# Kernel optimization log

Measured on AMD Instinct MI355X. Metric: run time of the kernel, lower is better.

The kernel has to match this reference:

```python
import jax, jax.numpy as jnp
import numpy as np

N_HEADS = 4

def setup_inputs() -> dict:
    key = jax.random.key(0)
    ks = jax.random.split(key, 9)
    B, C, H, W = 4, 256, 64, 64
    nh, hs = N_HEADS, C // N_HEADS
    s = 0.02
    return {
        "x": jax.random.normal(ks[0], (B, C, H, W), jnp.float32),
        "wq": jax.random.normal(ks[1], (C, C), jnp.float32) * s,
        "bq": jax.random.normal(ks[2], (C,), jnp.float32) * s,
        "wk": jax.random.normal(ks[3], (C, C), jnp.float32) * s,
        "bk": jax.random.normal(ks[4], (C,), jnp.float32) * s,
        "wv": jax.random.normal(ks[5], (C, C), jnp.float32) * s,
        "bv": jax.random.normal(ks[6], (C,), jnp.float32) * s,
        "rel_h": jax.random.normal(ks[7], (1, nh, hs, 1, H), jnp.float32),
        "rel_w": jax.random.normal(ks[8], (1, nh, hs, W, 1), jnp.float32),
    }

def reference(x, wq, bq, wk, bk, wv, bv, rel_h, rel_w):
    B, C, H, W = x.shape
    nh = N_HEADS
    hs = C // nh
    S = H * W

    def proj(w, b):
        # 1x1 conv == per-pixel linear over channels -> [B, C, H, W]
        y = jnp.einsum('oc,bchw->bohw', w, x) + b[None, :, None, None]
        # faithful to torch .view: flatten [C,H,W] row-major into [S, nh, hs]
        y = y.reshape(B, S, nh, hs)
        return y.transpose(0, 2, 1, 3)  # [B, nh, S, hs]

    q = proj(wq, bq)
    k = proj(wk, bk)
    v = proj(wv, bv)

    # content scores (NOTE: no 1/sqrt(d) scaling in BoT override)
    attn_content = jnp.einsum('bnqd,bnkd->bnqk', q, k)  # [B, nh, S, S]
    # learned relative position term: broadcast-add then flatten (w,h) order
    pos = (rel_h + rel_w).reshape(1, nh, hs, S)  # [1, nh, hs, S]
    attn_position = jnp.einsum('bnqd,ands->bnqs', q, pos)  # [B, nh, S, S]

    probs = jax.nn.softmax(attn_content + attn_position, axis=-1)
    ctx = jnp.einsum('bnqk,bnkd->bnqd', probs, v)  # [B, nh, S, hs]
    # faithful to torch: transpose(1,2) then view(B, C, width, height)
    out = ctx.transpose(0, 2, 1, 3).reshape(B, C, W, H)
    return out
```

## Files before the change

### kernel.cpp

```cpp
#include <hip/hip_runtime.h>
#include <hip/hip_bf16.h>
#include <stdint.h>
#include <math.h>

typedef __bf16 bf16_t;
typedef __bf16 bf16x8 __attribute__((ext_vector_type(8)));
typedef float  f32x4  __attribute__((ext_vector_type(4)));
typedef float  f32x16 __attribute__((ext_vector_type(16)));
typedef unsigned int u32;

#define S_SZ 4096
#define HS   64
#define OUT_B_STRIDE (256 * 64 * 64)
#define LOG2E 1.4426950408889634f

#define GLOAD_LDS(gsrc, ldst)                                                              \
    __builtin_amdgcn_global_load_lds((__attribute__((address_space(1))) void*)(void*)(gsrc), \
                                     (__attribute__((address_space(3))) void*)(void*)(ldst),  \
                                     16, 0, 0)

static __device__ __forceinline__ u32 pack2(__bf16 a, __bf16 b) {
    return (u32)__builtin_bit_cast(uint16_t, a) | ((u32)__builtin_bit_cast(uint16_t, b) << 16);
}

__global__ __launch_bounds__(256)
void prep_kernel(const float* __restrict__ wq, const float* __restrict__ wk,
                 const float* __restrict__ wv, const float* __restrict__ rel_h,
                 const float* __restrict__ rel_w,
                 bf16_t* __restrict__ Wh, bf16_t* __restrict__ Wl,
                 bf16_t* __restrict__ Rt)
{
    const int blk = blockIdx.x;
    if (blk < 48) {
        const int base = blk * 4096;
        #pragma unroll
        for (int i = 0; i < 16; ++i) {
            const int e = base + i * 256 + threadIdx.x;
            const int o = e >> 8, c = e & 255;
            const float* src = o < 256 ? wq : (o < 512 ? wk : wv);
            float v = src[(size_t)(o & 255) * 256 + c];
            if (o < 256) v *= LOG2E;
            __bf16 h = (__bf16)v;
            Wh[e] = h;
            Wl[e] = (__bf16)(v - (float)h);
        }
    } else {
        const int rb = blk - 48;
        const int n = rb >> 4, h2 = rb & 15;
        __shared__ float rh[4096], rw[4096];
        for (int i = threadIdx.x; i < 4096; i += 256) {
            rh[i] = rel_h[n * 4096 + i];
            rw[i] = rel_w[n * 4096 + i];
        }
        __syncthreads();
        bf16_t* Rp = Rt + ((size_t)n * 4096 + h2 * 256) * 64;
        const int d0 = (threadIdx.x & 7) * 8;
        const int ob = threadIdx.x >> 3;
        #pragma unroll
        for (int i = 0; i < 8; ++i) {
            const int o  = i * 32 + ob;
            const int ih = (o & 3) * 16 + h2;
            const int iw = o >> 2;
            bf16x8 rv;
            #pragma unroll
            for (int dd = 0; dd < 8; ++dd)
                rv[dd] = (bf16_t)(rh[(d0 + dd) * 64 + ih] + rw[(d0 + dd) * 64 + iw]);
            *(bf16x8*)(Rp + (size_t)o * 64 + d0) = rv;
        }
    }
}

__global__ __launch_bounds__(512, 2)
void proj_kernel(const float* __restrict__ x,
                 const bf16_t* __restrict__ Wh, const bf16_t* __restrict__ Wl,
                 const float* __restrict__ bq, const float* __restrict__ bk,
                 const float* __restrict__ bv, const bf16_t* __restrict__ Rt,
                 bf16_t* __restrict__ q_ws, bf16_t* __restrict__ k2_ws,
                 bf16_t* __restrict__ vt2_ws)
{
    const int bx = blockIdx.x;
    const int b  = bx >> 6;
    const int h  = bx & 63;
    const int p0 = h * 64;
    const int n  = h & 3;
    const int h2 = h >> 2;
    const int bn = b * 4 + n;
    const int tid = threadIdx.x;

    __shared__ __align__(16) char SM[65536];

    {
        const int cpair = tid & 127, pg = tid >> 7;
        const int c0 = cpair * 2;
        const float* x0 = x + ((size_t)b * 256 + c0) * 4096 + p0 + pg * 16;
        const int sub = (c0 >> 6) * 128;
        const int u   = (c0 >> 3) & 7;
        const int e2  = (c0 & 7) * 2;
        #pragma unroll
        for (int i4 = 0; i4 < 4; ++i4) {
            f32x4 ra = *(const f32x4*)(x0 + i4 * 4);
            f32x4 rb = *(const f32x4*)(x0 + 4096 + i4 * 4);
            #pragma unroll
            for (int i = 0; i < 4; ++i) {
                const int p = pg * 16 + i4 * 4 + i;
                __bf16 ha = (__bf16)ra[i], hb = (__bf16)rb[i];
                float  la = ra[i] - (float)ha, lb = rb[i] - (float)hb;
                const int off = p * 512 + sub + ((u ^ (p & 7)) * 16) + e2;
                *(u32*)(SM + off)         = pack2(ha, hb);
                *(u32*)(SM + 32768 + off) = pack2((__bf16)la, (__bf16)lb);
            }
        }
    }
    __syncthreads();

    const int wid = tid >> 6, lane = tid & 63, l31 = lane & 31, hi = lane >> 5;

    int obs[3], pjs[3];
    const bf16_t* whp[3];
    const bf16_t* wlp[3];
    #pragma unroll
    for (int j = 0; j < 3; ++j) {
        const int of = (wid * 3 + j) * 32;
        pjs[j] = of >> 8;
        obs[j] = of & 255;
        whp[j] = Wh + (size_t)(of + l31) * 256 + hi * 8;
        wlp[j] = Wl + (size_t)(of + l31) * 256 + hi * 8;
    }

    const char* XHp = SM + l31 * 512;
    const char* XLp = SM + 32768 + l31 * 512;

    f32x16 acc[3][2] = {};

    bf16x8 whC[3], wlC[3], whN[3], wlN[3];
    #pragma unroll
    for (int j = 0; j < 3; ++j) {
        whC[j] = *(const bf16x8*)(whp[j]);
        wlC[j] = *(const bf16x8*)(wlp[j]);
    }

    #pragma unroll
    for (int ks = 0; ks < 16; ++ks) {
        if (ks < 15) {
            #pragma unroll
            for (int j = 0; j < 3; ++j) {
                whN[j] = *(const bf16x8*)(whp[j] + (ks + 1) * 16);
                wlN[j] = *(const bf16x8*)(wlp[j] + (ks + 1) * 16);
            }
        }
        const int rb_ = (ks >> 2) * 128 + ((((ks * 2 + hi) & 7) ^ (l31 & 7)) * 16);
        bf16x8 xh[2], xl[2];
        #pragma unroll
        for (int pt = 0; pt < 2; ++pt) {
            xh[pt] = *(const bf16x8*)(XHp + pt * 16384 + rb_);
            xl[pt] = *(const bf16x8*)(XLp + pt * 16384 + rb_);
        }
        #pragma unroll
        for (int j = 0; j < 3; ++j)
            #pragma unroll
            for (int pt = 0; pt < 2; ++pt) {
                acc[j][pt] = __builtin_amdgcn_mfma_f32_32x32x16_bf16(whC[j], xh[pt], acc[j][pt], 0, 0, 0);
                acc[j][pt] = __builtin_amdgcn_mfma_f32_32x32x16_bf16(whC[j], xl[pt], acc[j][pt], 0, 0, 0);
                acc[j][pt] = __builtin_amdgcn_mfma_f32_32x32x16_bf16(wlC[j], xh[pt], acc[j][pt], 0, 0, 0);
            }
        #pragma unroll
        for (int j = 0; j < 3; ++j) { whC[j] = whN[j]; wlC[j] = wlN[j]; }
    }
    __syncthreads();

    f32x4 bias[3][2][4];
    #pragma unroll
    for (int j = 0; j < 3; ++j) {
        const float* bp = pjs[j] == 0 ? bq : (pjs[j] == 1 ? bk : bv);
        #pragma unroll
        for (int g2 = 0; g2 < 4; ++g2) {
            f32x4 v = *(const f32x4*)(bp + obs[j] + hi * 4 + g2 * 8);
            if (pjs[j] == 0) {
                #pragma unroll
                for (int i = 0; i < 4; ++i) v[i] *= LOG2E;
            }
            bias[j][0][g2] = v;  bias[j][1][g2] = v;
        }
    }

    #pragma unroll
    for (int j = 0; j < 3; ++j) {
        if (pjs[j] == 1) continue;
        #pragma unroll
        for (int pt = 0; pt < 2; ++pt) {
            const int d = pt * 32 + l31;
            #pragma unroll
            for (int g2 = 0; g2 < 4; ++g2)
                #pragma unroll
                for (int rr = 0; rr < 4; ++rr) {
                    const int o = obs[j] + rr + 4 * hi + 8 * g2;
                    const float v = acc[j][pt][g2 * 4 + rr] + bias[j][pt][g2][rr];
                    if (pjs[j] == 0) {
                        *(bf16_t*)(SM + o * 128 + d * 2) = (bf16_t)v;
                    } else {
                        *(bf16_t*)(SM + 32768 + d * 512 + ((o * 2) ^ ((d & 7) << 4))) = (bf16_t)v;
                    }
                }
        }
    }
    __syncthreads();
    {
        bf16_t* qp = q_ws + (size_t)bn * 4096 * 64;
        #pragma unroll
        for (int i = 0; i < 4; ++i) {
            const int c = i * 512 + tid;
            const int o = c >> 3, d8 = c & 7;
            uint4 v = *(const uint4*)(SM + c * 16);
            *(uint4*)(qp + (size_t)(o * 16 + h2) * 64 + d8 * 8) = v;
        }
        bf16_t* vp = vt2_ws + (size_t)bn * 64 * 4096 + h2 * 256;
        #pragma unroll
        for (int i = 0; i < 4; ++i) {
            const int c = i * 512 + tid;
            const int d = c >> 5, k = c & 31;
            uint4 v = *(const uint4*)(SM + 32768 + d * 512 + ((k * 16) ^ ((d & 7) << 4)));
            *(uint4*)(vp + (size_t)d * 4096 + k * 8) = v;
        }
    }
    __syncthreads();

    #pragma unroll
    for (int j = 0; j < 3; ++j) {
        if (pjs[j] != 1) continue;
        #pragma unroll
        for (int pt = 0; pt < 2; ++pt) {
            const int d = pt * 32 + l31;
            #pragma unroll
            for (int g2 = 0; g2 < 4; ++g2)
                #pragma unroll
                for (int rr = 0; rr < 4; ++rr) {
                    const int o = obs[j] + rr + 4 * hi + 8 * g2;
                    *(bf16_t*)(SM + o * 128 + d * 2) =
                        (bf16_t)(acc[j][pt][g2 * 4 + rr] + bias[j][pt][g2][rr]);
                }
        }
    }
    __syncthreads();
    {
        const bf16_t* Rp = Rt + ((size_t)n * 4096 + h2 * 256) * 64;
        bf16_t* kp = k2_ws + ((size_t)bn * 4096 + h2 * 256) * 64;
        #pragma unroll
        for (int i = 0; i < 4; ++i) {
            const int c = i * 512 + tid;
            bf16x8 kv = *(const bf16x8*)(SM + c * 16);
            bf16x8 rv = *(const bf16x8*)(Rp + c * 8);
            bf16x8 res;
            #pragma unroll
            for (int ii = 0; ii < 8; ++ii)
                res[ii] = (__bf16)((float)kv[ii] + (float)rv[ii]);
            *(bf16x8*)(kp + c * 8) = res;
        }
    }
}

__global__ __launch_bounds__(256, 2)
void attn_kernel(const bf16_t* __restrict__ q_ws, const bf16_t* __restrict__ k_ws,
                 const bf16_t* __restrict__ vt_ws, float* __restrict__ out)
{
    const int tid  = threadIdx.x;
    const int wid  = tid >> 6;
    const int lane = tid & 63;
    const int l31  = lane & 31;
    const int hi   = lane >> 5;

    const int wg  = blockIdx.x;
    const int swz = (wg & 7) * 64 + (wg >> 3);
    const int bn  = swz >> 5;
    const int qb  = swz & 31;
    const int b   = bn >> 2, n = bn & 3;

    __shared__ __align__(16) bf16_t Kt[4][64 * 64];
    __shared__ __align__(16) bf16_t Vt[4][64 * 64];

    const bf16_t* Qb = q_ws  + (size_t)bn * S_SZ * HS;
    const bf16_t* Kb = k_ws  + (size_t)bn * S_SZ * HS;
    const bf16_t* Vb = vt_ws + (size_t)bn * HS * S_SZ;

    const int c0 = wid * 64 + lane;
    const int ra = c0 >> 3, ga = (c0 & 7) ^ (ra & 7);
    const bf16_t* ksrcA = Kb + ra * HS + ga * 8;
    const bf16_t* ksrcB = ksrcA + 32 * HS;
    const bf16_t* vsrcA = Vb + (size_t)ra * S_SZ + ga * 8;
    const bf16_t* vsrcB = vsrcA + (size_t)32 * S_SZ;

#define STAGE(buf, ts)                                                        \
    GLOAD_LDS(ksrcA + (size_t)(ts) * 64 * HS, &Kt[buf][wid * 512]);           \
    GLOAD_LDS(ksrcB + (size_t)(ts) * 64 * HS, &Kt[buf][2048 + wid * 512]);    \
    GLOAD_LDS(vsrcA + (ts) * 64,              &Vt[buf][wid * 512]);           \
    GLOAD_LDS(vsrcB + (ts) * 64,              &Vt[buf][2048 + wid * 512]);

    const int q = qb * 128 + wid * 32 + l31;
    bf16x8 qf[4];
    #pragma unroll
    for (int dk = 0; dk < 4; ++dk)
        qf[dk] = *(const bf16x8*)(Qb + (size_t)q * HS + dk * 16 + hi * 8);

    f32x16 oacc[2];
    f32x16 Z16;
    #pragma unroll
    for (int i = 0; i < 16; ++i) { oacc[0][i] = 0.f; oacc[1][i] = 0.f; Z16[i] = 0.f; }
    float lsum = 0.f;

    const int swzme = (l31 & 7) << 4;

#define QKPAIR(DST, BUF)                                                               \
    { const char* Kb_ = (const char*)&Kt[BUF][0] + l31 * 128;                          \
      __builtin_amdgcn_s_setprio(1);                                                   \
      _Pragma("unroll")                                                                \
      for (int hh = 0; hh < 2; ++hh) {                                                 \
          bf16x8 kf[4];                                                                \
          _Pragma("unroll")                                                            \
          for (int dk = 0; dk < 4; ++dk)                                               \
              kf[dk] = *(const bf16x8*)(Kb_ + hh * 4096 + (((2 * dk + hi) * 16) ^ swzme)); \
          DST[hh] = __builtin_amdgcn_mfma_f32_32x32x16_bf16(kf[0], qf[0], Z16, 0, 0, 0);   \
          _Pragma("unroll")                                                            \
          for (int dk = 1; dk < 4; ++dk)                                               \
              DST[hh] = __builtin_amdgcn_mfma_f32_32x32x16_bf16(kf[dk], qf[dk], DST[hh], 0, 0, 0); \
      }                                                                                \
      __builtin_amdgcn_s_setprio(0); }

#define EXPPV(SRC, VBUF)                                                               \
    { u32 Wd[2][4][2];                                                                 \
      float ps[4] = {0.f, 0.f, 0.f, 0.f};                                              \
      _Pragma("unroll")                                                                \
      for (int hh = 0; hh < 2; ++hh)                                                   \
      _Pragma("unroll")                                                                \
      for (int c = 0; c < 4; ++c)                                                      \
      _Pragma("unroll")                                                                \
      for (int tt = 0; tt < 2; ++tt) {                                                 \
          float pa = __builtin_amdgcn_exp2f(SRC[hh][c * 4 + tt * 2]);                  \
          float pb = __builtin_amdgcn_exp2f(SRC[hh][c * 4 + tt * 2 + 1]);              \
          ps[c] += pa + pb;                                                            \
          u32 w_;                                                                      \
          asm("v_cvt_pk_bf16_f32 %0, %1, %2" : "=v"(w_) : "v"(pa), "v"(pb));           \
          Wd[hh][c][tt] = w_; }                                                        \
      lsum += (ps[0] + ps[1]) + (ps[2] + ps[3]);                                       \
      u32 F[4][4];                                                                     \
      _Pragma("unroll")                                                                \
      for (int hh = 0; hh < 2; ++hh)                                                   \
      _Pragma("unroll")                                                                \
      for (int pr = 0; pr < 2; ++pr)                                                   \
      _Pragma("unroll")                                                                \
      for (int tt = 0; tt < 2; ++tt) {                                                 \
          u32 a_ = Wd[hh][2 * pr][tt], b_ = Wd[hh][2 * pr + 1][tt];                    \
          asm("v_permlane32_swap_b32 %0, %1" : "+v"(a_), "+v"(b_));                    \
          F[2 * hh + pr][tt]     = a_;                                                 \
          F[2 * hh + pr][2 + tt] = b_; }                                               \
      const char* Vb_ = (const char*)&Vt[VBUF][0] + l31 * 128;                         \
      __builtin_amdgcn_s_setprio(1);                                                   \
      _Pragma("unroll")                                                                \
      for (int dh = 0; dh < 2; ++dh)                                                   \
      _Pragma("unroll")                                                                \
      for (int kk = 0; kk < 4; ++kk) {                                                 \
          bf16x8 vf = *(const bf16x8*)(Vb_ + dh * 4096 + (((2 * kk + hi) * 16) ^ swzme)); \
          union { u32 u[4]; bf16x8 v; } pf;                                            \
          pf.u[0] = F[kk][0]; pf.u[1] = F[kk][1]; pf.u[2] = F[kk][2]; pf.u[3] = F[kk][3]; \
          oacc[dh] = __builtin_amdgcn_mfma_f32_32x32x16_bf16(vf, pf.v, oacc[dh], 0, 0, 0); } \
      __builtin_amdgcn_s_setprio(0); }

#define ITER(U, SC, SN)                                                                \
    { asm volatile("s_waitcnt vmcnt(4)" ::: "memory");                                 \
      __builtin_amdgcn_s_barrier();                                                    \
      asm volatile("" ::: "memory");                                                   \
      { const int t_ = tb + (U);                                                       \
        const int ts_ = (t_ + 3 > 63) ? 63 : t_ + 3;                                   \
        STAGE(((U) + 3) & 3, ts_); }                                                   \
      QKPAIR(SN, ((U) + 1) & 3);                                                       \
      EXPPV(SC, (U) & 3); }

    STAGE(0, 0); STAGE(1, 1); STAGE(2, 2);
    asm volatile("s_waitcnt vmcnt(8)" ::: "memory");
    __builtin_amdgcn_s_barrier();
    asm volatile("" ::: "memory");

    f32x16 S0[2], S1[2];
    QKPAIR(S0, 0);

    for (int tb = 0; tb < 64; tb += 4) {
        ITER(0, S0, S1);
        ITER(1, S1, S0);
        ITER(2, S0, S1);
        ITER(3, S1, S0);
    }
#undef ITER
#undef EXPPV
#undef QKPAIR
#undef STAGE

    float lt  = lsum + __shfl_xor(lsum, 32);
    float inv = 1.0f / lt;
    float* outp = out + (size_t)b * OUT_B_STRIDE + (size_t)q * 256 + n * 64;
    #pragma unroll
    for (int dh = 0; dh < 2; ++dh)
        #pragma unroll
        for (int g2 = 0; g2 < 4; ++g2) {
            f32x4 v4;
            #pragma unroll
            for (int r = 0; r < 4; ++r) v4[r] = oacc[dh][g2 * 4 + r] * inv;
            *(f32x4*)(outp + dh * 32 + g2 * 8 + hi * 4) = v4;
        }
}

extern "C" void kernel_launch(void* const* d_in, const int* in_sizes, int n_in,
                              void* d_out, int out_size, void* d_ws, size_t ws_size,
                              hipStream_t stream)
{
    const float* x     = (const float*)d_in[0];
    const float* wq    = (const float*)d_in[1];
    const float* bq    = (const float*)d_in[2];
    const float* wk    = (const float*)d_in[3];
    const float* bk    = (const float*)d_in[4];
    const float* wv    = (const float*)d_in[5];
    const float* bv    = (const float*)d_in[6];
    const float* rel_h = (const float*)d_in[7];
    const float* rel_w = (const float*)d_in[8];
    float* out = (float*)d_out;

    bf16_t* q_ws   = (bf16_t*)d_ws;
    bf16_t* k2_ws  = q_ws  + (size_t)16 * S_SZ * HS;
    bf16_t* vt2_ws = k2_ws + (size_t)16 * S_SZ * HS;

    bf16_t* end = (bf16_t*)d_out + (size_t)out_size * 2;
    bf16_t* Wl  = end - 196608;
    bf16_t* Wh  = Wl - 196608;
    bf16_t* Rt  = Wh - 1048576;

    prep_kernel<<<112, 256, 0, stream>>>(wq, wk, wv, rel_h, rel_w, Wh, Wl, Rt);
    proj_kernel<<<256, 512, 0, stream>>>(x, Wh, Wl, bq, bk, bv, Rt,
                                         q_ws, k2_ws, vt2_ws);
    attn_kernel<<<512, 256, 0, stream>>>(q_ws, k2_ws, vt2_ws, out);
}
```

Measured before the change: 127.7 us.

## Process two 32-query tiles per wave to reuse K/V fragments across queries

Each wave now handles 64 queries (two 32-row MFMA tiles), so each K and V fragment loaded from LDS feeds two MFMAs. The workgroup count drops from 512 to 256 and launch bounds go to one block per SIMD set. The software pipeline that overlapped the next tile's QK with the current exp/PV, along with the setprio hints, is replaced by a simpler per-tile sequence with the barrier moved to after compute. Register pressure rises a lot, occupancy falls, and 256 workgroups may underfill the 256 CUs.

Result: slower. 138.4 us (+8.4%).

```diff
diff --git a/kernel.cpp b/kernel.cpp
--- a/kernel.cpp
+++ b/kernel.cpp
@@ -258,7 +258,7 @@
     }
 }
 
-__global__ __launch_bounds__(256, 2)
+__global__ __launch_bounds__(256, 1)
 void attn_kernel(const bf16_t* __restrict__ q_ws, const bf16_t* __restrict__ k_ws,
                  const bf16_t* __restrict__ vt_ws, float* __restrict__ out)
 {
@@ -269,9 +269,9 @@
     const int hi   = lane >> 5;
 
     const int wg  = blockIdx.x;
-    const int swz = (wg & 7) * 64 + (wg >> 3);
-    const int bn  = swz >> 5;
-    const int qb  = swz & 31;
+    const int swz = (wg & 7) * 32 + (wg >> 3);
+    const int bn  = swz >> 4;
+    const int qb  = swz & 15;
     const int b   = bn >> 2, n = bn & 3;
 
     __shared__ __align__(16) bf16_t Kt[4][64 * 64];
@@ -294,115 +294,143 @@
     GLOAD_LDS(vsrcA + (ts) * 64,              &Vt[buf][wid * 512]);           \
     GLOAD_LDS(vsrcB + (ts) * 64,              &Vt[buf][2048 + wid * 512]);
 
-    const int q = qb * 128 + wid * 32 + l31;
-    bf16x8 qf[4];
-    #pragma unroll
-    for (int dk = 0; dk < 4; ++dk)
-        qf[dk] = *(const bf16x8*)(Qb + (size_t)q * HS + dk * 16 + hi * 8);
-
-    f32x16 oacc[2];
+    const int q0 = qb * 256 + wid * 64 + l31;
+    bf16x8 qf0[4], qf1[4];
+    #pragma unroll
+    for (int dk = 0; dk < 4; ++dk) {
+        qf0[dk] = *(const bf16x8*)(Qb + (size_t)q0 * HS + dk * 16 + hi * 8);
+        qf1[dk] = *(const bf16x8*)(Qb + (size_t)(q0 + 32) * HS + dk * 16 + hi * 8);
+    }
+
+    f32x16 oacc[2][2];
     f32x16 Z16;
     #pragma unroll
-    for (int i = 0; i < 16; ++i) { oacc[0][i] = 0.f; oacc[1][i] = 0.f; Z16[i] = 0.f; }
-    float lsum = 0.f;
+    for (int i = 0; i < 16; ++i) {
+        oacc[0][0][i] = 0.f; oacc[0][1][i] = 0.f;
+        oacc[1][0][i] = 0.f; oacc[1][1][i] = 0.f;
+        Z16[i] = 0.f;
+    }
+    float lsum0 = 0.f, lsum1 = 0.f;
 
     const int swzme = (l31 & 7) << 4;
 
-#define QKPAIR(DST, BUF)                                                               \
+#define TILE(BUF)                                                                      \
     { const char* Kb_ = (const char*)&Kt[BUF][0] + l31 * 128;                          \
-      __builtin_amdgcn_s_setprio(1);                                                   \
+      const char* Vb_ = (const char*)&Vt[BUF][0] + l31 * 128;                          \
+      f32x16 sacc[2][2];                                                               \
       _Pragma("unroll")                                                                \
       for (int hh = 0; hh < 2; ++hh) {                                                 \
           bf16x8 kf[4];                                                                \
           _Pragma("unroll")                                                            \
           for (int dk = 0; dk < 4; ++dk)                                               \
               kf[dk] = *(const bf16x8*)(Kb_ + hh * 4096 + (((2 * dk + hi) * 16) ^ swzme)); \
-          DST[hh] = __builtin_amdgcn_mfma_f32_32x32x16_bf16(kf[0], qf[0], Z16, 0, 0, 0);   \
+          sacc[hh][0] = __builtin_amdgcn_mfma_f32_32x32x16_bf16(kf[0], qf0[0], Z16, 0, 0, 0); \
+          sacc[hh][1] = __builtin_amdgcn_mfma_f32_32x32x16_bf16(kf[0], qf1[0], Z16, 0, 0, 0); \
           _Pragma("unroll")                                                            \
-          for (int dk = 1; dk < 4; ++dk)                                               \
-              DST[hh] = __builtin_amdgcn_mfma_f32_32x32x16_bf16(kf[dk], qf[dk], DST[hh], 0, 0, 0); \
+          for (int dk = 1; dk < 4; ++dk) {                                             \
+              sacc[hh][0] = __builtin_amdgcn_mfma_f32_32x32x16_bf16(kf[dk], qf0[dk], sacc[hh][0], 0, 0, 0); \
+              sacc[hh][1] = __builtin_amdgcn_mfma_f32_32x32x16_bf16(kf[dk], qf1[dk], sacc[hh][1], 0, 0, 0); \
+          }                                                                            \
       }                                                                                \
-      __builtin_amdgcn_s_setprio(0); }
-
-#define EXPPV(SRC, VBUF)                                                               \
-    { u32 Wd[2][4][2];                                                                 \
-      float ps[4] = {0.f, 0.f, 0.f, 0.f};                                              \
-      _Pragma("unroll")                                                                \
-      for (int hh = 0; hh < 2; ++hh)                                                   \
-      _Pragma("unroll")                                                                \
-      for (int c = 0; c < 4; ++c)                                                      \
-      _Pragma("unroll")                                                                \
-      for (int tt = 0; tt < 2; ++tt) {                                                 \
-          float pa = __builtin_amdgcn_exp2f(SRC[hh][c * 4 + tt * 2]);                  \
-          float pb = __builtin_amdgcn_exp2f(SRC[hh][c * 4 + tt * 2 + 1]);              \
-          ps[c] += pa + pb;                                                            \
-          u32 w_;                                                                      \
-          asm("v_cvt_pk_bf16_f32 %0, %1, %2" : "=v"(w_) : "v"(pa), "v"(pb));           \
-          Wd[hh][c][tt] = w_; }                                                        \
-      lsum += (ps[0] + ps[1]) + (ps[2] + ps[3]);                                       \
-      u32 F[4][4];                                                                     \
-      _Pragma("unroll")                                                                \
-      for (int hh = 0; hh < 2; ++hh)                                                   \
-      _Pragma("unroll")                                                                \
-      for (int pr = 0; pr < 2; ++pr)                                                   \
-      _Pragma("unroll")                                                                \
-      for (int tt = 0; tt < 2; ++tt) {                                                 \
-          u32 a_ = Wd[hh][2 * pr][tt], b_ = Wd[hh][2 * pr + 1][tt];                    \
-          asm("v_permlane32_swap_b32 %0, %1" : "+v"(a_), "+v"(b_));                    \
-          F[2 * hh + pr][tt]     = a_;                                                 \
-          F[2 * hh + pr][2 + tt] = b_; }                                               \
-      const char* Vb_ = (const char*)&Vt[VBUF][0] + l31 * 128;                         \
-      __builtin_amdgcn_s_setprio(1);                                                   \
+      u32 F0[4][4], F1[4][4];                                                          \
+      { u32 Wd[2][4][2];                                                               \
+        float ps[4] = {0.f, 0.f, 0.f, 0.f};                                            \
+        _Pragma("unroll")                                                              \
+        for (int hh = 0; hh < 2; ++hh)                                                 \
+        _Pragma("unroll")                                                              \
+        for (int c = 0; c < 4; ++c)                                                    \
+        _Pragma("unroll")                                                              \
+        for (int tt = 0; tt < 2; ++tt) {                                               \
+            float pa = __builtin_amdgcn_exp2f(sacc[hh][0][c * 4 + tt * 2]);            \
+            float pb = __builtin_amdgcn_exp2f(sacc[hh][0][c * 4 + tt * 2 + 1]);        \
+            ps[c] += pa + pb;                                                          \
+            u32 w_;                                                                    \
+            asm("v_cvt_pk_bf16_f32 %0, %1, %2" : "=v"(w_) : "v"(pa), "v"(pb));         \
+            Wd[hh][c][tt] = w_; }                                                      \
+        lsum0 += (ps[0] + ps[1]) + (ps[2] + ps[3]);                                    \
+        _Pragma("unroll")                                                              \
+        for (int hh = 0; hh < 2; ++hh)                                                 \
+        _Pragma("unroll")                                                              \
+        for (int pr = 0; pr < 2; ++pr)                                                 \
+        _Pragma("unroll")                                                              \
+        for (int tt = 0; tt < 2; ++tt) {                                               \
+            u32 a_ = Wd[hh][2 * pr][tt], b_ = Wd[hh][2 * pr + 1][tt];                  \
+            asm("v_permlane32_swap_b32 %0, %1" : "+v"(a_), "+v"(b_));                  \
+            F0[2 * hh + pr][tt]     = a_;                                              \
+            F0[2 * hh + pr][2 + tt] = b_; } }                                          \
+      { u32 Wd[2][4][2];                                                               \
+        float ps[4] = {0.f, 0.f, 0.f, 0.f};                                            \
+        _Pragma("unroll")                                                              \
+        for (int hh = 0; hh < 2; ++hh)                                                 \
+        _Pragma("unroll")                                                              \
+        for (int c = 0; c < 4; ++c)                                                    \
+        _Pragma("unroll")                                                              \
+        for (int tt = 0; tt < 2; ++tt) {                                               \
+            float pa = __builtin_amdgcn_exp2f(sacc[hh][1][c * 4 + tt * 2]);            \
+            float pb = __builtin_amdgcn_exp2f(sacc[hh][1][c * 4 + tt * 2 + 1]);        \
+            ps[c] += pa + pb;                                                          \
+            u32 w_;                                                                    \
+            asm("v_cvt_pk_bf16_f32 %0, %1, %2" : "=v"(w_) : "v"(pa), "v"(pb));         \
+            Wd[hh][c][tt] = w_; }                                                      \
+        lsum1 += (ps[0] + ps[1]) + (ps[2] + ps[3]);                                    \
+        _Pragma("unroll")                                                              \
+        for (int hh = 0; hh < 2; ++hh)                                                 \
+        _Pragma("unroll")                                                              \
+        for (int pr = 0; pr < 2; ++pr)                                                 \
+        _Pragma("unroll")                                                              \
+        for (int tt = 0; tt < 2; ++tt) {                                               \
+            u32 a_ = Wd[hh][2 * pr][tt], b_ = Wd[hh][2 * pr + 1][tt];                  \
+            asm("v_permlane32_swap_b32 %0, %1" : "+v"(a_), "+v"(b_));                  \
+            F1[2 * hh + pr][tt]     = a_;                                              \
+            F1[2 * hh + pr][2 + tt] = b_; } }                                          \
       _Pragma("unroll")                                                                \
       for (int dh = 0; dh < 2; ++dh)                                                   \
       _Pragma("unroll")                                                                \
       for (int kk = 0; kk < 4; ++kk) {                                                 \
           bf16x8 vf = *(const bf16x8*)(Vb_ + dh * 4096 + (((2 * kk + hi) * 16) ^ swzme)); \
-          union { u32 u[4]; bf16x8 v; } pf;                                            \
-          pf.u[0] = F[kk][0]; pf.u[1] = F[kk][1]; pf.u[2] = F[kk][2]; pf.u[3] = F[kk][3]; \
-          oacc[dh] = __builtin_amdgcn_mfma_f32_32x32x16_bf16(vf, pf.v, oacc[dh], 0, 0, 0); } \
-      __builtin_amdgcn_s_setprio(0); }
-
-#define ITER(U, SC, SN)                                                                \
-    { asm volatile("s_waitcnt vmcnt(4)" ::: "memory");                                 \
-      __builtin_amdgcn_s_barrier();                                                    \
-      asm volatile("" ::: "memory");                                                   \
-      { const int t_ = tb + (U);                                                       \
-        const int ts_ = (t_ + 3 > 63) ? 63 : t_ + 3;                                   \
-        STAGE(((U) + 3) & 3, ts_); }                                                   \
-      QKPAIR(SN, ((U) + 1) & 3);                                                       \
-      EXPPV(SC, (U) & 3); }
+          union { u32 u[4]; bf16x8 v; } p0, p1;                                        \
+          p0.u[0] = F0[kk][0]; p0.u[1] = F0[kk][1]; p0.u[2] = F0[kk][2]; p0.u[3] = F0[kk][3]; \
+          p1.u[0] = F1[kk][0]; p1.u[1] = F1[kk][1]; p1.u[2] = F1[kk][2]; p1.u[3] = F1[kk][3]; \
+          oacc[dh][0] = __builtin_amdgcn_mfma_f32_32x32x16_bf16(vf, p0.v, oacc[dh][0], 0, 0, 0); \
+          oacc[dh][1] = __builtin_amdgcn_mfma_f32_32x32x16_bf16(vf, p1.v, oacc[dh][1], 0, 0, 0); } }
 
     STAGE(0, 0); STAGE(1, 1); STAGE(2, 2);
     asm volatile("s_waitcnt vmcnt(8)" ::: "memory");
     __builtin_amdgcn_s_barrier();
     asm volatile("" ::: "memory");
 
-    f32x16 S0[2], S1[2];
-    QKPAIR(S0, 0);
-
     for (int tb = 0; tb < 64; tb += 4) {
-        ITER(0, S0, S1);
-        ITER(1, S1, S0);
-        ITER(2, S0, S1);
-        ITER(3, S1, S0);
-    }
-#undef ITER
-#undef EXPPV
-#undef QKPAIR
+        #pragma unroll
+        for (int u = 0; u < 4; ++u) {
+            const int t = tb + u;
+            { const int ts = (t + 3 > 63) ? 63 : t + 3; STAGE((u + 3) & 3, ts); }
+            TILE(u);
+            asm volatile("s_waitcnt vmcnt(4)" ::: "memory");
+            __builtin_amdgcn_s_barrier();
+            asm volatile("" ::: "memory");
+        }
+    }
+#undef TILE
 #undef STAGE
 
-    float lt  = lsum + __shfl_xor(lsum, 32);
-    float inv = 1.0f / lt;
-    float* outp = out + (size_t)b * OUT_B_STRIDE + (size_t)q * 256 + n * 64;
+    float lt0 = lsum0 + __shfl_xor(lsum0, 32);
+    float lt1 = lsum1 + __shfl_xor(lsum1, 32);
+    float inv0 = 1.0f / lt0;
+    float inv1 = 1.0f / lt1;
+    float* outp0 = out + (size_t)b * OUT_B_STRIDE + (size_t)q0 * 256 + n * 64;
+    float* outp1 = outp0 + 32 * 256;
     #pragma unroll
     for (int dh = 0; dh < 2; ++dh)
         #pragma unroll
         for (int g2 = 0; g2 < 4; ++g2) {
-            f32x4 v4;
-            #pragma unroll
-            for (int r = 0; r < 4; ++r) v4[r] = oacc[dh][g2 * 4 + r] * inv;
-            *(f32x4*)(outp + dh * 32 + g2 * 8 + hi * 4) = v4;
+            f32x4 v4, w4;
+            #pragma unroll
+            for (int r = 0; r < 4; ++r) {
+                v4[r] = oacc[dh][0][g2 * 4 + r] * inv0;
+                w4[r] = oacc[dh][1][g2 * 4 + r] * inv1;
+            }
+            *(f32x4*)(outp0 + dh * 32 + g2 * 8 + hi * 4) = v4;
+            *(f32x4*)(outp1 + dh * 32 + g2 * 8 + hi * 4) = w4;
         }
 }
 
@@ -433,5 +461,5 @@
     prep_kernel<<<112, 256, 0, stream>>>(wq, wk, wv, rel_h, rel_w, Wh, Wl, Rt);
     proj_kernel<<<256, 512, 0, stream>>>(x, Wh, Wl, bq, bk, bv, Rt,
                                          q_ws, k2_ws, vt2_ws);
-    attn_kernel<<<512, 256, 0, stream>>>(q_ws, k2_ws, vt2_ws, out);
+    attn_kernel<<<256, 256, 0, stream>>>(q_ws, k2_ws, vt2_ws, out);
 }
```

## Replace software-pipelined QK/PV loop with two-tile-per-barrier schedule

Applied to the files above, without the earlier changes.

Drops the cross-iteration software pipeline, where the next tile's QK^T ran before the current tile's exp and PV. Each K/V tile is now handled start to finish (QK, exp, PV) inside one macro. Two tiles are processed per barrier, with the next two tiles staged into LDS and a full vmcnt(0) wait at the end of each pair. This halves the barriers and frees the registers for the second score buffer, but gives up the overlap between QK MFMAs and the exp/permute work, and the full drain may expose load latency.

New measurement: 130.6 us. 2.3% more time.

```diff
diff --git a/kernel.cpp b/kernel.cpp
--- a/kernel.cpp
+++ b/kernel.cpp
@@ -308,8 +308,10 @@
 
     const int swzme = (l31 & 7) << 4;
 
-#define QKPAIR(DST, BUF)                                                               \
+#define TILE(BUF)                                                                      \
     { const char* Kb_ = (const char*)&Kt[BUF][0] + l31 * 128;                          \
+      const char* Vb_ = (const char*)&Vt[BUF][0] + l31 * 128;                          \
+      f32x16 sacc[2];                                                                  \
       __builtin_amdgcn_s_setprio(1);                                                   \
       _Pragma("unroll")                                                                \
       for (int hh = 0; hh < 2; ++hh) {                                                 \
@@ -317,15 +319,13 @@
           _Pragma("unroll")                                                            \
           for (int dk = 0; dk < 4; ++dk)                                               \
               kf[dk] = *(const bf16x8*)(Kb_ + hh * 4096 + (((2 * dk + hi) * 16) ^ swzme)); \
-          DST[hh] = __builtin_amdgcn_mfma_f32_32x32x16_bf16(kf[0], qf[0], Z16, 0, 0, 0);   \
+          sacc[hh] = __builtin_amdgcn_mfma_f32_32x32x16_bf16(kf[0], qf[0], Z16, 0, 0, 0);  \
           _Pragma("unroll")                                                            \
           for (int dk = 1; dk < 4; ++dk)                                               \
-              DST[hh] = __builtin_amdgcn_mfma_f32_32x32x16_bf16(kf[dk], qf[dk], DST[hh], 0, 0, 0); \
+              sacc[hh] = __builtin_amdgcn_mfma_f32_32x32x16_bf16(kf[dk], qf[dk], sacc[hh], 0, 0, 0); \
       }                                                                                \
-      __builtin_amdgcn_s_setprio(0); }
-
-#define EXPPV(SRC, VBUF)                                                               \
-    { u32 Wd[2][4][2];                                                                 \
+      __builtin_amdgcn_s_setprio(0);                                                   \
+      u32 Wd[2][4][2];                                                                 \
       float ps[4] = {0.f, 0.f, 0.f, 0.f};                                              \
       _Pragma("unroll")                                                                \
       for (int hh = 0; hh < 2; ++hh)                                                   \
@@ -333,8 +333,8 @@
       for (int c = 0; c < 4; ++c)                                                      \
       _Pragma("unroll")                                                                \
       for (int tt = 0; tt < 2; ++tt) {                                                 \
-          float pa = __builtin_amdgcn_exp2f(SRC[hh][c * 4 + tt * 2]);                  \
-          float pb = __builtin_amdgcn_exp2f(SRC[hh][c * 4 + tt * 2 + 1]);              \
+          float pa = __builtin_amdgcn_exp2f(sacc[hh][c * 4 + tt * 2]);                 \
+          float pb = __builtin_amdgcn_exp2f(sacc[hh][c * 4 + tt * 2 + 1]);             \
           ps[c] += pa + pb;                                                            \
           u32 w_;                                                                      \
           asm("v_cvt_pk_bf16_f32 %0, %1, %2" : "=v"(w_) : "v"(pa), "v"(pb));           \
@@ -351,7 +351,6 @@
           asm("v_permlane32_swap_b32 %0, %1" : "+v"(a_), "+v"(b_));                    \
           F[2 * hh + pr][tt]     = a_;                                                 \
           F[2 * hh + pr][2 + tt] = b_; }                                               \
-      const char* Vb_ = (const char*)&Vt[VBUF][0] + l31 * 128;                         \
       __builtin_amdgcn_s_setprio(1);                                                   \
       _Pragma("unroll")                                                                \
       for (int dh = 0; dh < 2; ++dh)                                                   \
@@ -363,33 +362,23 @@
           oacc[dh] = __builtin_amdgcn_mfma_f32_32x32x16_bf16(vf, pf.v, oacc[dh], 0, 0, 0); } \
       __builtin_amdgcn_s_setprio(0); }
 
-#define ITER(U, SC, SN)                                                                \
-    { asm volatile("s_waitcnt vmcnt(4)" ::: "memory");                                 \
-      __builtin_amdgcn_s_barrier();                                                    \
-      asm volatile("" ::: "memory");                                                   \
-      { const int t_ = tb + (U);                                                       \
-        const int ts_ = (t_ + 3 > 63) ? 63 : t_ + 3;                                   \
-        STAGE(((U) + 3) & 3, ts_); }                                                   \
-      QKPAIR(SN, ((U) + 1) & 3);                                                       \
-      EXPPV(SC, (U) & 3); }
-
-    STAGE(0, 0); STAGE(1, 1); STAGE(2, 2);
-    asm volatile("s_waitcnt vmcnt(8)" ::: "memory");
+    STAGE(0, 0); STAGE(1, 1);
+    asm volatile("s_waitcnt vmcnt(0)" ::: "memory");
     __builtin_amdgcn_s_barrier();
     asm volatile("" ::: "memory");
 
-    f32x16 S0[2], S1[2];
-    QKPAIR(S0, 0);
-
-    for (int tb = 0; tb < 64; tb += 4) {
-        ITER(0, S0, S1);
-        ITER(1, S1, S0);
-        ITER(2, S0, S1);
-        ITER(3, S1, S0);
-    }
-#undef ITER
-#undef EXPPV
-#undef QKPAIR
+    for (int t = 0; t < 64; t += 2) {
+        { const int t2 = (t + 2 < 64) ? t + 2 : 63;
+          const int t3 = (t + 3 < 64) ? t + 3 : 63;
+          STAGE((t + 2) & 3, t2);
+          STAGE((t + 3) & 3, t3); }
+        TILE(t & 3);
+        TILE((t + 1) & 3);
+        asm volatile("s_waitcnt vmcnt(0)" ::: "memory");
+        __builtin_amdgcn_s_barrier();
+        asm volatile("" ::: "memory");
+    }
+#undef TILE
 #undef STAGE
 
     float lt  = lsum + __shfl_xor(lsum, 32);
```
